# Performance work log

Measured on AMD Instinct MI355X. Metric: run time of the kernel, lower is better.

The kernel has to match this reference:

```python
import jax, jax.numpy as jnp
import numpy as np

N_WIDTH = 8
N_ORDER = 2
N_ELEMENTS = 1024
N_NODES = N_ELEMENTS * N_ORDER + 1  # 2049
N_SAMPLES = 4096
X_MIN = 0.0
X_MAX = 1.0


def _ref_nodes():
    return np.linspace(-1.0, 1.0, N_ORDER + 1)


def _lagrange(x):
    # x: [I, K] -> [I, K, P]
    nodes = _ref_nodes()
    cols = []
    for j in range(N_ORDER + 1):
        p = jnp.ones_like(x)
        for m in range(N_ORDER + 1):
            if j != m:
                p = p * (x - nodes[m]) / (nodes[j] - nodes[m])
        cols.append(p)
    return jnp.stack(cols, axis=-1)


def _dlagrange(x):
    nodes = _ref_nodes()
    cols = []
    for j in range(N_ORDER + 1):
        y = jnp.zeros_like(x)
        for i in range(N_ORDER + 1):
            if i != j:
                k = jnp.ones_like(x) / (nodes[j] - nodes[i])
                for m in range(N_ORDER + 1):
                    if m != i and m != j:
                        k = k * (x - nodes[m]) / (nodes[j] - nodes[m])
                y = y + k
        cols.append(y)
    return jnp.stack(cols, axis=-1)


def _ddlagrange(x):
    nodes = _ref_nodes()
    cols = []
    for j in range(N_ORDER + 1):
        y = jnp.zeros_like(x)
        for i in range(N_ORDER + 1):
            if i != j:
                k_sum = jnp.zeros_like(x)
                for m in range(N_ORDER + 1):
                    if m != i and m != j:
                        k_prod = jnp.ones_like(x) / (nodes[j] - nodes[m])
                        for n in range(N_ORDER + 1):
                            if n != i and n != j and n != m:
                                k_prod = k_prod * (x - nodes[n]) / (nodes[j] - nodes[n])
                        k_sum = k_sum + k_prod
                y = y + (1.0 / (nodes[j] - nodes[i])) * k_sum
        cols.append(y)
    return jnp.stack(cols, axis=-1)


def setup_inputs() -> dict:
    key = jax.random.key(0)
    k1, k2 = jax.random.split(key)
    x = jax.random.uniform(k1, (N_SAMPLES,), dtype=jnp.float32)  # in [x_min, x_max)
    weight = jax.random.normal(k2, (N_WIDTH, N_NODES), dtype=jnp.float32) * 0.02
    return {"x": x, "weight": weight}


def reference(x, weight):
    # replicate 1-D input across width: [I] -> [I, K]
    x2 = jnp.repeat(x[:, None], N_WIDTH, axis=-1)
    x_shift = (N_NODES - 1) * (x2 - X_MIN) / (X_MAX - X_MIN)
    id_el = jnp.clip(jnp.floor(x_shift / N_ORDER), 0, N_ELEMENTS - 1)
    nodes_l = (id_el * N_ORDER).astype(jnp.int32)  # [I, K]
    nodes_lf = jax.lax.stop_gradient(nodes_l.astype(x_shift.dtype))
    # reference coord: (x_shift - 0.5*(l + r)) / (0.5*(r - l)) with r = l + n_order
    x_t = (x_shift - (nodes_lf + 0.5 * N_ORDER)) / (0.5 * N_ORDER)

    delta_x = 0.5 * N_ORDER * (X_MAX - X_MIN) / (N_NODES - 1)
    phi_loc = _lagrange(x_t)                       # [I, K, P]
    dphi_loc = _dlagrange(x_t) / delta_x
    ddphi_loc = _ddlagrange(x_t) / (delta_x * delta_x)

    I, K = x2.shape
    P = N_ORDER + 1
    idx = nodes_l[:, :, None] + jnp.arange(P)      # [I, K, P] global node ids
    ii = jnp.arange(I)[:, None, None]
    kk = jnp.arange(K)[None, :, None]
    phi_ikp = jnp.zeros((I, K, N_NODES), x2.dtype).at[ii, kk, idx].set(phi_loc)
    dphi_ikp = jnp.zeros((I, K, N_NODES), x2.dtype).at[ii, kk, idx].set(dphi_loc)
    ddphi_ikp = jnp.zeros((I, K, N_NODES), x2.dtype).at[ii, kk, idx].set(ddphi_loc)

    t_ik = jnp.einsum('kp,ikp->ik', weight, phi_ikp)
    dt_ik = jnp.einsum('kp,ikp->ik', weight, dphi_ikp)
    ddt_ik = jnp.einsum('kp,ikp->ik', weight, ddphi_ikp)
    return (t_ik, dt_ik, ddt_ik, phi_ikp, dphi_ikp, ddphi_ikp)
```

## Files before the change

kernel.cpp:

```cpp
#include <hip/hip_runtime.h>


#define KN_WIDTH    8
#define KN_NODES    2049
#define KN_SAMPLES  4096
#define KN_IK       (KN_SAMPLES * KN_WIDTH)
#define KN_HEAD     (3 * KN_IK)
#define KN_PHI_LEN  ((size_t)KN_IK * KN_NODES)

__device__ __forceinline__ void kann_coord(float xv, int& nl, float& x_t) {
    float xs  = 2048.0f * xv;
    float fid = floorf(0.5f * xs);
    fid = fminf(fmaxf(fid, 0.0f), 1023.0f);
    nl  = 2 * (int)fid;
    x_t = xs - ((float)nl + 1.0f);
}

__global__ __launch_bounds__(256)
void KANN_head(const float* __restrict__ x, const float* __restrict__ w,
               float* __restrict__ out) {
    int ik = blockIdx.x * 256 + threadIdx.x;
    if (ik >= KN_IK) return;
    int i = ik >> 3, k = ik & 7;
    int nl; float x_t; kann_coord(x[i], nl, x_t);
    float p0 = 0.5f * x_t * (x_t - 1.0f);
    float p1 = 1.0f - x_t * x_t;
    float p2 = 0.5f * x_t * (x_t + 1.0f);
    const float s = 2048.0f, s2 = 2048.0f * 2048.0f;
    const float* wk = w + k * KN_NODES + nl;
    float w0 = wk[0], w1 = wk[1], w2 = wk[2];
    out[ik]             = w0 * p0 + w1 * p1 + w2 * p2;
    out[KN_IK + ik]     = (w0 * (x_t - 0.5f) - 2.0f * w1 * x_t + w2 * (x_t + 0.5f)) * s;
    out[2 * KN_IK + ik] = (w0 - 2.0f * w1 + w2) * s2;
}

__global__ __launch_bounds__(256)
void KANN_body(const float* __restrict__ x, float* __restrict__ out) {
    const int y = blockIdx.y;
    float* base = out + KN_HEAD + (size_t)y * KN_PHI_LEN;
    const unsigned nf4 = (unsigned)(KN_PHI_LEN / 4);
    const unsigned stride = gridDim.x * blockDim.x;

    for (unsigned f4 = blockIdx.x * blockDim.x + threadIdx.x; f4 < nf4; f4 += stride) {
        unsigned e0   = f4 * 4u;
        unsigned row  = e0 / KN_NODES;
        unsigned col0 = e0 - row * KN_NODES;
        float vv[4] = {0.0f, 0.0f, 0.0f, 0.0f};

        if (col0 < KN_NODES - 3) {
            int i = (int)(row >> 3);
            int nl; float x_t; kann_coord(x[i], nl, x_t);
            int d0 = (int)col0 - nl;
            if (d0 >= -3 && d0 <= 2) {
                float b0, b1, b2;
                if (y == 0)      { b0 = 0.5f * x_t * (x_t - 1.0f); b1 = 1.0f - x_t * x_t; b2 = 0.5f * x_t * (x_t + 1.0f); }
                else if (y == 1) { b0 = (x_t - 0.5f) * 2048.0f; b1 = -4096.0f * x_t; b2 = (x_t + 0.5f) * 2048.0f; }
                else             { b0 = 4194304.0f; b1 = -8388608.0f; b2 = 4194304.0f; }
#pragma unroll
                for (int j = 0; j < 4; ++j) {
                    int d = d0 + j;
                    vv[j] = (d == 0) ? b0 : ((d == 1) ? b1 : ((d == 2) ? b2 : 0.0f));
                }
            }
        } else {
#pragma unroll
            for (int j = 0; j < 4; ++j) {
                unsigned e = e0 + j;
                unsigned r = e / KN_NODES;
                unsigned c = e - r * KN_NODES;
                int i = (int)(r >> 3);
                int nl; float x_t; kann_coord(x[i], nl, x_t);
                int d = (int)c - nl;
                if (d >= 0 && d <= 2) {
                    float b;
                    if (y == 0)      b = (d == 0) ? 0.5f * x_t * (x_t - 1.0f) : ((d == 1) ? 1.0f - x_t * x_t : 0.5f * x_t * (x_t + 1.0f));
                    else if (y == 1) b = ((d == 0) ? (x_t - 0.5f) : ((d == 1) ? (-2.0f * x_t) : (x_t + 0.5f))) * 2048.0f;
                    else             b = (d == 1) ? -8388608.0f : 4194304.0f;
                    vv[j] = b;
                }
            }
        }
        float4 v = make_float4(vv[0], vv[1], vv[2], vv[3]);
        *reinterpret_cast<float4*>(base + (size_t)e0) = v;
    }
}

extern "C" void kernel_launch(void* const* d_in, const int* in_sizes, int n_in,
                              void* d_out, int out_size, void* d_ws, size_t ws_size,
                              hipStream_t stream) {
    const float* x = (const float*)d_in[0];
    const float* w = (const float*)d_in[1];
    float* out = (float*)d_out;

    KANN_head<<<dim3(KN_IK / 256), dim3(256), 0, stream>>>(x, w, out);
    KANN_body<<<dim3(1024, 3), dim3(256), 0, stream>>>(x, out);
}
```

Baseline: 161.7 us.

## Fuse head and body kernels into one per-sample block kernel with fast zero path

Merges the two kernels into a single launch in which each block handles one sample's 8xNODES slab for one output tensor. Computing x, nl and x_t once per block removes the per-element integer division and the repeated x loads. A wave-uniform branch lets most float4 stores write zeros directly. This saves one launch and per-element index arithmetic, but the grid grows to 12288 blocks, each doing a short loop.

```diff
diff --git a/kernel.cpp b/kernel.cpp
--- a/kernel.cpp
+++ b/kernel.cpp
@@ -1,87 +1,68 @@
 #include <hip/hip_runtime.h>
 
 
-#define KN_WIDTH    8
 #define KN_NODES    2049
 #define KN_SAMPLES  4096
-#define KN_IK       (KN_SAMPLES * KN_WIDTH)
+#define KN_IK       (KN_SAMPLES * 8)
 #define KN_HEAD     (3 * KN_IK)
 #define KN_PHI_LEN  ((size_t)KN_IK * KN_NODES)
+#define KN_ROWF     (8 * KN_NODES)
+#define KN_NF4      (KN_ROWF / 4)
 
-__device__ __forceinline__ void kann_coord(float xv, int& nl, float& x_t) {
+__global__ __launch_bounds__(256)
+void KANN_all(const float* __restrict__ x, const float* __restrict__ w,
+              float* __restrict__ out) {
+    const int i = blockIdx.x;
+    const int y = blockIdx.y;
+
+    float xv  = x[i];
     float xs  = 2048.0f * xv;
     float fid = floorf(0.5f * xs);
     fid = fminf(fmaxf(fid, 0.0f), 1023.0f);
-    nl  = 2 * (int)fid;
-    x_t = xs - ((float)nl + 1.0f);
-}
+    int   nl  = 2 * (int)fid;
+    float x_t = xs - (float)nl - 1.0f;
 
-__global__ __launch_bounds__(256)
-void KANN_head(const float* __restrict__ x, const float* __restrict__ w,
-               float* __restrict__ out) {
-    int ik = blockIdx.x * 256 + threadIdx.x;
-    if (ik >= KN_IK) return;
-    int i = ik >> 3, k = ik & 7;
-    int nl; float x_t; kann_coord(x[i], nl, x_t);
-    float p0 = 0.5f * x_t * (x_t - 1.0f);
-    float p1 = 1.0f - x_t * x_t;
-    float p2 = 0.5f * x_t * (x_t + 1.0f);
-    const float s = 2048.0f, s2 = 2048.0f * 2048.0f;
-    const float* wk = w + k * KN_NODES + nl;
-    float w0 = wk[0], w1 = wk[1], w2 = wk[2];
-    out[ik]             = w0 * p0 + w1 * p1 + w2 * p2;
-    out[KN_IK + ik]     = (w0 * (x_t - 0.5f) - 2.0f * w1 * x_t + w2 * (x_t + 0.5f)) * s;
-    out[2 * KN_IK + ik] = (w0 - 2.0f * w1 + w2) * s2;
-}
+    float b0, b1, b2;
+    if (y == 0)      { b0 = 0.5f * x_t * (x_t - 1.0f); b1 = 1.0f - x_t * x_t; b2 = 0.5f * x_t * (x_t + 1.0f); }
+    else if (y == 1) { b0 = (x_t - 0.5f) * 2048.0f; b1 = -4096.0f * x_t; b2 = (x_t + 0.5f) * 2048.0f; }
+    else             { b0 = 4194304.0f; b1 = -8388608.0f; b2 = 4194304.0f; }
 
-__global__ __launch_bounds__(256)
-void KANN_body(const float* __restrict__ x, float* __restrict__ out) {
-    const int y = blockIdx.y;
-    float* base = out + KN_HEAD + (size_t)y * KN_PHI_LEN;
-    const unsigned nf4 = (unsigned)(KN_PHI_LEN / 4);
-    const unsigned stride = gridDim.x * blockDim.x;
+    if (y == 0 && threadIdx.x < 8) {
+        int k = threadIdx.x;
+        const float* wk = w + k * KN_NODES + nl;
+        float w0 = wk[0], w1 = wk[1], w2 = wk[2];
+        float p0 = 0.5f * x_t * (x_t - 1.0f);
+        float p1 = 1.0f - x_t * x_t;
+        float p2 = 0.5f * x_t * (x_t + 1.0f);
+        int ik = i * 8 + k;
+        out[ik]             = w0 * p0 + w1 * p1 + w2 * p2;
+        out[KN_IK + ik]     = (w0 * (x_t - 0.5f) - 2.0f * w1 * x_t + w2 * (x_t + 0.5f)) * 2048.0f;
+        out[2 * KN_IK + ik] = (w0 - 2.0f * w1 + w2) * 4194304.0f;
+    }
 
-    for (unsigned f4 = blockIdx.x * blockDim.x + threadIdx.x; f4 < nf4; f4 += stride) {
-        unsigned e0   = f4 * 4u;
-        unsigned row  = e0 / KN_NODES;
-        unsigned col0 = e0 - row * KN_NODES;
-        float vv[4] = {0.0f, 0.0f, 0.0f, 0.0f};
+    float* base = out + KN_HEAD + (size_t)y * KN_PHI_LEN + (size_t)i * KN_ROWF;
+    const float4 zero4 = make_float4(0.0f, 0.0f, 0.0f, 0.0f);
 
-        if (col0 < KN_NODES - 3) {
-            int i = (int)(row >> 3);
-            int nl; float x_t; kann_coord(x[i], nl, x_t);
-            int d0 = (int)col0 - nl;
-            if (d0 >= -3 && d0 <= 2) {
-                float b0, b1, b2;
-                if (y == 0)      { b0 = 0.5f * x_t * (x_t - 1.0f); b1 = 1.0f - x_t * x_t; b2 = 0.5f * x_t * (x_t + 1.0f); }
-                else if (y == 1) { b0 = (x_t - 0.5f) * 2048.0f; b1 = -4096.0f * x_t; b2 = (x_t + 0.5f) * 2048.0f; }
-                else             { b0 = 4194304.0f; b1 = -8388608.0f; b2 = 4194304.0f; }
-#pragma unroll
-                for (int j = 0; j < 4; ++j) {
-                    int d = d0 + j;
-                    vv[j] = (d == 0) ? b0 : ((d == 1) ? b1 : ((d == 2) ? b2 : 0.0f));
-                }
-            }
-        } else {
+    for (int f = threadIdx.x; f < KN_NF4; f += 256) {
+        int e0 = f << 2;
+        int r  = e0 >> 11;
+        int c  = (e0 & 2047) - r;
+        if (c < 0) { r -= 1; c += KN_NODES; }
+        int  d0   = c - nl;
+        bool hot  = (d0 >= -3 && d0 <= 2) || (c >= 2046 && nl <= 2);
+        if (__builtin_expect(__any(hot), 0)) {
+            float vv[4];
 #pragma unroll
             for (int j = 0; j < 4; ++j) {
-                unsigned e = e0 + j;
-                unsigned r = e / KN_NODES;
-                unsigned c = e - r * KN_NODES;
-                int i = (int)(r >> 3);
-                int nl; float x_t; kann_coord(x[i], nl, x_t);
-                int d = (int)c - nl;
-                if (d >= 0 && d <= 2) {
-                    float b;
-                    if (y == 0)      b = (d == 0) ? 0.5f * x_t * (x_t - 1.0f) : ((d == 1) ? 1.0f - x_t * x_t : 0.5f * x_t * (x_t + 1.0f));
-                    else if (y == 1) b = ((d == 0) ? (x_t - 0.5f) : ((d == 1) ? (-2.0f * x_t) : (x_t + 0.5f))) * 2048.0f;
-                    else             b = (d == 1) ? -8388608.0f : 4194304.0f;
-                    vv[j] = b;
-                }
+                int cj = c + j;
+                if (cj > 2048) cj -= KN_NODES;
+                int d = cj - nl;
+                vv[j] = (d == 0) ? b0 : ((d == 1) ? b1 : ((d == 2) ? b2 : 0.0f));
             }
+            *reinterpret_cast<float4*>(base + e0) = make_float4(vv[0], vv[1], vv[2], vv[3]);
+        } else {
+            *reinterpret_cast<float4*>(base + e0) = zero4;
         }
-        float4 v = make_float4(vv[0], vv[1], vv[2], vv[3]);
-        *reinterpret_cast<float4*>(base + (size_t)e0) = v;
     }
 }
 
@@ -91,7 +72,5 @@
     const float* x = (const float*)d_in[0];
     const float* w = (const float*)d_in[1];
     float* out = (float*)d_out;
-
-    KANN_head<<<dim3(KN_IK / 256), dim3(256), 0, stream>>>(x, w, out);
-    KANN_body<<<dim3(1024, 3), dim3(256), 0, stream>>>(x, out);
+    KANN_all<<<dim3(KN_SAMPLES, 3), dim3(256), 0, stream>>>(x, w, out);
 }
```

Result: slower. 168.8 us (+4.4%).
